# Kernel tuning notes

Measured on AMD Instinct MI355X. Metric: run time of the kernel, lower is better.

## Reference

```python
import jax, jax.numpy as jnp
import numpy as np

B, N, FIN, FOUT, H = 4, 2048, 256, 256, 4
D = FOUT // H  # out_per_head


def setup_inputs() -> dict:
    key = jax.random.key(0)
    k1, k2, k3, k4 = jax.random.split(key, 4)
    h = jax.random.normal(k1, (B, N, FIN), dtype=jnp.float32)
    adj = jax.random.randint(k2, (B, N, N), 0, 2, dtype=jnp.int32)
    idx = jnp.arange(N)
    adj = adj.at[:, idx, idx].set(1)  # self-loops: avoid empty softmax rows
    W = jax.random.normal(k3, (FOUT, FIN), dtype=jnp.float32) / np.sqrt(FIN)
    attn = jax.random.normal(k4, (H, 2 * D), dtype=jnp.float32) * 0.1
    return {"h": h, "adj": adj, "W": W, "attn": attn}


def reference(h, adj, W, attn):
    Bb, Nn, _ = h.shape
    Hh = attn.shape[0]
    d = attn.shape[1] // 2
    # h_proj: [B, H, N, d]  (nn.Linear with no bias: h @ W.T)
    hp = (h @ W.T).reshape(Bb, Nn, Hh, d).transpose(0, 2, 1, 3)
    # attn . concat(h_i, h_j) == (a_src . h_i) + (a_dst . h_j); avoids O(N^2 * 2d) concat
    a_src, a_dst = attn[:, :d], attn[:, d:]
    s = jnp.einsum('bhnd,hd->bhn', hp, a_src)  # score contribution of row node i
    t = jnp.einsum('bhnd,hd->bhn', hp, a_dst)  # score contribution of col node j
    e = jax.nn.leaky_relu(s[:, :, :, None] + t[:, :, None, :], negative_slope=0.2)
    e = jnp.where(adj[:, None, :, :] != 0, e, -jnp.inf)
    alpha = jax.nn.softmax(e, axis=-1)  # [B, H, N, N]
    h_new = jnp.einsum('bhij,bhjd->bhid', alpha, hp)
    h_new = h_new.transpose(0, 2, 1, 3).reshape(Bb, Nn, Hh * d)
    return h_new, alpha.mean(axis=1)
```

## Files before the change

### kernel.cpp

```cpp
#include <hip/hip_runtime.h>
#include <math.h>

typedef unsigned long long u64;
typedef unsigned short ushort_t;
typedef float f32x4 __attribute__((ext_vector_type(4)));
typedef short short8 __attribute__((ext_vector_type(8)));

#define BB 4
#define NN 2048
#define FINE 256
#define FOUTE 256
#define HH 4
#define DD 64
#define NW 32
#define L2E 1.44269504088896340736f

#define EXP2F(x) __builtin_amdgcn_exp2f(x)
#define LOG2F(x) __builtin_amdgcn_logf(x)

__device__ __forceinline__ float lrelu(float x) { return fmaxf(x, 0.2f * x); }

__device__ __forceinline__ unsigned short f2bf(float x) {
  unsigned u = __float_as_uint(x);
  unsigned r = u + 0x7FFFu + ((u >> 16) & 1u);
  return (unsigned short)(r >> 16);
}

__device__ __forceinline__ unsigned cvtpk(float lo, float hi) {
  unsigned r;
  asm("v_cvt_pk_bf16_f32 %0, %1, %2" : "=v"(r) : "v"(lo), "v"(hi));
  return r;
}

__global__ __launch_bounds__(256) void k_pack(const int* __restrict__ adj, u64* __restrict__ pack,
                                              float4* __restrict__ outZero) {
  int row = blockIdx.x;
  if (row < 2048) outZero[(size_t)row * 256 + threadIdx.x] = make_float4(0.f, 0.f, 0.f, 0.f);
  int wv = threadIdx.x >> 6, ln = threadIdx.x & 63;
  const int* arow = adj + (size_t)row * NN;
  u64* prow = pack + (size_t)row * NW;
  for (int w = wv; w < NW; w += 4) {
    u64 m = __ballot(arow[(w << 6) + ln] != 0);
    if (ln == 0) prow[w] = m;
  }
}

__global__ __launch_bounds__(256) void k_gemm1(const float* __restrict__ hI, const float* __restrict__ W,
                                               const float* __restrict__ attn,
                                               ushort_t* __restrict__ hpT,
                                               float* __restrict__ sB, float* __restrict__ tB,
                                               float* __restrict__ tB4) {
  __shared__ ushort_t Ab[64 * 256];
  __shared__ ushort_t Bb[64 * 256];
  __shared__ ushort_t tT[64][72];
  int m0 = blockIdx.x * 64;
  int hh = blockIdx.y;
  int f0 = hh * 64;
  int tid = threadIdx.x;
  int w = tid >> 6, lane = tid & 63;
  int li = lane & 15, g = lane >> 4;

#pragma unroll
  for (int q = 0; q < 16; ++q) {
    int fi = (q << 8) + tid;
    int row = fi >> 6, f4 = fi & 63;
    float4 va = *(const float4*)&hI[(size_t)(m0 + row) * FINE + (f4 << 2)];
    float4 vb = *(const float4*)&W[(size_t)(f0 + row) * FINE + (f4 << 2)];
    int byteOff = (row << 9) + ((f4 << 3) ^ ((row & 7) << 4));
    *(uint2*)((char*)Ab + byteOff) = make_uint2(cvtpk(va.x, va.y), cvtpk(va.z, va.w));
    *(uint2*)((char*)Bb + byteOff) = make_uint2(cvtpk(vb.x, vb.y), cvtpk(vb.z, vb.w));
  }
  __syncthreads();

  f32x4 acc[4] = {};
  int arow = (w << 4) + li;
  int abase = arow << 9, asw = (arow & 7) << 4;
#pragma unroll
  for (int kk = 0; kk < 8; ++kk) {
    short8 a = *(const short8*)((char*)Ab + abase + (((kk << 6) + (g << 4)) ^ asw));
#pragma unroll
    for (int f = 0; f < 4; ++f) {
      int brow = (f << 4) + li;
      short8 b = *(const short8*)((char*)Bb + (brow << 9) + (((kk << 6) + (g << 4)) ^ ((brow & 7) << 4)));
      acc[f] = __builtin_amdgcn_mfma_f32_16x16x32_bf16(a, b, acc[f], 0, 0, 0);
    }
  }

  float as4[4], ad4[4];
#pragma unroll
  for (int f = 0; f < 4; ++f) {
    as4[f] = attn[(hh << 7) + (f << 4) + li] * L2E;
    ad4[f] = attn[(hh << 7) + 64 + (f << 4) + li] * L2E;
  }
  float ps[4] = {0.f, 0.f, 0.f, 0.f}, pt[4] = {0.f, 0.f, 0.f, 0.f};
#pragma unroll
  for (int f = 0; f < 4; ++f)
#pragma unroll
    for (int r = 0; r < 4; ++r) { ps[r] += acc[f][r] * as4[f]; pt[r] += acc[f][r] * ad4[f]; }
#pragma unroll
  for (int off = 1; off <= 8; off <<= 1) {
#pragma unroll
    for (int r = 0; r < 4; ++r) { ps[r] += __shfl_xor(ps[r], off); pt[r] += __shfl_xor(pt[r], off); }
  }
  int b0 = m0 >> 11, n0 = m0 & (NN - 1);
  if (li == 0) {
#pragma unroll
    for (int r = 0; r < 4; ++r) {
      int nn = n0 + (w << 4) + (g << 2) + r;
      size_t idx = (size_t)(b0 * HH + hh) * NN + nn;
      sB[idx] = ps[r]; tB[idx] = pt[r];
      tB4[((size_t)b0 * NN + nn) * 4 + hh] = pt[r];
    }
  }
#pragma unroll
  for (int f = 0; f < 4; ++f)
#pragma unroll
    for (int r = 0; r < 4; ++r)
      tT[(f << 4) + li][(w << 4) + (g << 2) + r] = f2bf(acc[f][r]);
  __syncthreads();
#pragma unroll
  for (int q = 0; q < 2; ++q) {
    int dr = (q << 5) + (tid >> 3);
    int seg = tid & 7;
    *(short8*)&hpT[((size_t)((b0 * HH + hh) << 6) + dr) * NN + n0 + (seg << 3)] =
        *(const short8*)&tT[dr][seg << 3];
  }
}

__global__ __launch_bounds__(256) void k_mls(const float* __restrict__ sB, const float* __restrict__ tB4,
                                             const u64* __restrict__ pack, float* __restrict__ cB,
                                             float* __restrict__ outMean) {
  __shared__ float4 t4s[2048];
  __shared__ float4 wpart[4];
  int tid = threadIdx.x;
  int lane = tid & 63;
  int wv = tid >> 6;
  int bbase = blockIdx.x << 3;
  int b = bbase >> 11;
  const float4* t4 = (const float4*)tB4 + (size_t)b * NN;
#pragma unroll
  for (int q = 0; q < 8; ++q) t4s[(q << 8) + tid] = t4[(q << 8) + tid];
  __syncthreads();

  float4 pm = make_float4(-1e30f, -1e30f, -1e30f, -1e30f);
#pragma unroll
  for (int q = 0; q < 8; ++q) {
    float4 tv = t4s[(wv << 9) + (q << 6) + lane];
    pm.x = fmaxf(pm.x, tv.x); pm.y = fmaxf(pm.y, tv.y);
    pm.z = fmaxf(pm.z, tv.z); pm.w = fmaxf(pm.w, tv.w);
  }
#pragma unroll
  for (int off = 32; off; off >>= 1) {
    pm.x = fmaxf(pm.x, __shfl_xor(pm.x, off));
    pm.y = fmaxf(pm.y, __shfl_xor(pm.y, off));
    pm.z = fmaxf(pm.z, __shfl_xor(pm.z, off));
    pm.w = fmaxf(pm.w, __shfl_xor(pm.w, off));
  }
  if (lane == 0) wpart[wv] = pm;
  __syncthreads();
  float4 q0 = wpart[0], q1 = wpart[1], q2 = wpart[2], q3 = wpart[3];
  float tmax[4] = {fmaxf(fmaxf(q0.x, q1.x), fmaxf(q2.x, q3.x)),
                   fmaxf(fmaxf(q0.y, q1.y), fmaxf(q2.y, q3.y)),
                   fmaxf(fmaxf(q0.z, q1.z), fmaxf(q2.z, q3.z)),
                   fmaxf(fmaxf(q0.w, q1.w), fmaxf(q2.w, q3.w))};

  int r0 = __builtin_amdgcn_readfirstlane(bbase + (wv << 1));
  const u64* p0 = pack + (size_t)(r0 + 0) * NW;
  const u64* p1 = pack + (size_t)(r0 + 1) * NW;
  float sv[2][4], Ah[2][4], Bh[2][4], mh[2][4];
#pragma unroll
  for (int r = 0; r < 2; ++r)
#pragma unroll
    for (int h = 0; h < 4; ++h) {
      float s = sB[(size_t)(b * HH + h) * NN + ((r0 + r) & (NN - 1))];
      float m = lrelu(s + tmax[h]);
      sv[r][h] = s; mh[r][h] = m; Ah[r][h] = s - m; Bh[r][h] = fmaf(0.2f, s, -m);
    }
  unsigned mr0 = 0, mr1 = 0;
  float4 ls0 = make_float4(0.f, 0.f, 0.f, 0.f), ls1 = ls0;
#pragma unroll 4
  for (int k = 0; k < NW; ++k) {
    bool b0 = (p0[k] >> lane) & 1ull, b1 = (p1[k] >> lane) & 1ull;
    mr0 |= (unsigned)b0 << k; mr1 |= (unsigned)b1 << k;
    float4 tv = t4s[(k << 6) + lane];
    ls0.x += b0 ? EXP2F(fmaxf(tv.x + Ah[0][0], fmaf(0.2f, tv.x, Bh[0][0]))) : 0.f;
    ls0.y += b0 ? EXP2F(fmaxf(tv.y + Ah[0][1], fmaf(0.2f, tv.y, Bh[0][1]))) : 0.f;
    ls0.z += b0 ? EXP2F(fmaxf(tv.z + Ah[0][2], fmaf(0.2f, tv.z, Bh[0][2]))) : 0.f;
    ls0.w += b0 ? EXP2F(fmaxf(tv.w + Ah[0][3], fmaf(0.2f, tv.w, Bh[0][3]))) : 0.f;
    ls1.x += b1 ? EXP2F(fmaxf(tv.x + Ah[1][0], fmaf(0.2f, tv.x, Bh[1][0]))) : 0.f;
    ls1.y += b1 ? EXP2F(fmaxf(tv.y + Ah[1][1], fmaf(0.2f, tv.y, Bh[1][1]))) : 0.f;
    ls1.z += b1 ? EXP2F(fmaxf(tv.z + Ah[1][2], fmaf(0.2f, tv.z, Bh[1][2]))) : 0.f;
    ls1.w += b1 ? EXP2F(fmaxf(tv.w + Ah[1][3], fmaf(0.2f, tv.w, Bh[1][3]))) : 0.f;
  }
#pragma unroll
  for (int off = 32; off; off >>= 1) {
    ls0.x += __shfl_xor(ls0.x, off); ls0.y += __shfl_xor(ls0.y, off);
    ls0.z += __shfl_xor(ls0.z, off); ls0.w += __shfl_xor(ls0.w, off);
    ls1.x += __shfl_xor(ls1.x, off); ls1.y += __shfl_xor(ls1.y, off);
    ls1.z += __shfl_xor(ls1.z, off); ls1.w += __shfl_xor(ls1.w, off);
  }
  float A2[2][4], B2[2][4];
  float lv0[4] = {ls0.x, ls0.y, ls0.z, ls0.w};
  float lv1[4] = {ls1.x, ls1.y, ls1.z, ls1.w};
#pragma unroll
  for (int h = 0; h < 4; ++h) {
    float c0 = mh[0][h] + LOG2F(lv0[h]);
    float c1 = mh[1][h] + LOG2F(lv1[h]);
    A2[0][h] = sv[0][h] - c0; B2[0][h] = fmaf(0.2f, sv[0][h], -c0);
    A2[1][h] = sv[1][h] - c1; B2[1][h] = fmaf(0.2f, sv[1][h], -c1);
    if (lane == 0) {
      cB[(size_t)(b * HH + h) * NN + ((r0 + 0) & (NN - 1))] = c0;
      cB[(size_t)(b * HH + h) * NN + ((r0 + 1) & (NN - 1))] = c1;
    }
  }
#pragma unroll 2
  for (int k = 0; k < NW; ++k) {
    float4 tv = t4s[(k << 6) + lane];
    float tvv[4] = {tv.x, tv.y, tv.z, tv.w};
    float a0 = 0.f, a1 = 0.f;
#pragma unroll
    for (int h = 0; h < 4; ++h) {
      a0 += EXP2F(fmaxf(tvv[h] + A2[0][h], fmaf(0.2f, tvv[h], B2[0][h])));
      a1 += EXP2F(fmaxf(tvv[h] + A2[1][h], fmaf(0.2f, tvv[h], B2[1][h])));
    }
    outMean[(size_t)(r0 + 0) * NN + (k << 6) + lane] = ((mr0 >> k) & 1u) ? 0.25f * a0 : 0.0f;
    outMean[(size_t)(r0 + 1) * NN + (k << 6) + lane] = ((mr1 >> k) & 1u) ? 0.25f * a1 : 0.0f;
  }
}

__global__ __launch_bounds__(256) void k_pv(const ushort_t* __restrict__ hpT,
                                            const float* __restrict__ sB, const float* __restrict__ cB,
                                            const float* __restrict__ tB, const u64* __restrict__ pack,
                                            float* __restrict__ out) {
  __shared__ ushort_t hpTile[2][4096];
  int blk = blockIdx.x;
  int jh = blockIdx.y;
  int it = blk & 31, bh = blk >> 5;
  int b = bh >> 2, hh = bh & 3;
  int i0 = it << 6;
  int tid = threadIdx.x;
  int w = tid >> 6, lane = tid & 63;
  int li = lane & 15, g = lane >> 4;
  int irow = i0 + (w << 4) + li;
  float sI = sB[(size_t)bh * NN + irow];
  float cI = cB[(size_t)bh * NN + irow];
  float A0 = sI - cI, B0 = fmaf(0.2f, sI, -cI);
  const u64* packRow = pack + ((size_t)b * NN + irow) * NW;
  const float* tRow = tB + (size_t)bh * NN;

  int drow0 = (w << 4) + (lane >> 3);
  int xslot = (lane & 7) ^ (lane >> 3);
  const ushort_t* srcBase0 = hpT + ((size_t)(bh << 6) + drow0) * NN + (xslot << 3);
  const ushort_t* srcBase1 = srcBase0 + (size_t)8 * NN;

#define STAGE(buf, j0c)                                                                        \
  do {                                                                                         \
    __builtin_amdgcn_global_load_lds(                                                          \
        (const __attribute__((address_space(1))) void*)(srcBase0 + (j0c)),                     \
        (__attribute__((address_space(3))) void*)&hpTile[buf][(w << 10)], 16, 0, 0);           \
    __builtin_amdgcn_global_load_lds(                                                          \
        (const __attribute__((address_space(1))) void*)(srcBase1 + (j0c)),                     \
        (__attribute__((address_space(3))) void*)&hpTile[buf][(w << 10) + 512], 16, 0, 0);     \
  } while (0)

  f32x4 acc[4] = {};
  int jc0 = jh << 4;
  STAGE(0, jc0 << 6);
  STAGE(1, (jc0 + 1) << 6);
  float4 ta0, ta1, tb0, tb1;
  u64 wbits;
  {
    const float4* tp4 = (const float4*)(tRow + (jc0 << 6) + (g << 3));
    ta0 = tp4[0]; ta1 = tp4[1]; tb0 = tp4[8]; tb1 = tp4[9];
    wbits = packRow[jc0];
  }
  int cur = 0;

  for (int jc = jc0; jc < jc0 + 16; ++jc) {
    float tva[8] = {ta0.x, ta0.y, ta0.z, ta0.w, ta1.x, ta1.y, ta1.z, ta1.w};
    float tvb[8] = {tb0.x, tb0.y, tb0.z, tb0.w, tb1.x, tb1.y, tb1.z, tb1.w};
    unsigned bits0 = (unsigned)(wbits >> (g << 3));
    unsigned bits1 = (unsigned)(wbits >> (32 + (g << 3)));
    float ea[8], eb[8];
#pragma unroll
    for (int jj = 0; jj < 8; ++jj) {
      float e0 = EXP2F(fmaxf(tva[jj] + A0, fmaf(0.2f, tva[jj], B0)));
      ea[jj] = ((bits0 >> jj) & 1u) ? e0 : 0.0f;
      float e1 = EXP2F(fmaxf(tvb[jj] + A0, fmaf(0.2f, tvb[jj], B0)));
      eb[jj] = ((bits1 >> jj) & 1u) ? e1 : 0.0f;
    }
    uint4 ua, ub;
    ua.x = cvtpk(ea[0], ea[1]); ua.y = cvtpk(ea[2], ea[3]);
    ua.z = cvtpk(ea[4], ea[5]); ua.w = cvtpk(ea[6], ea[7]);
    ub.x = cvtpk(eb[0], eb[1]); ub.y = cvtpk(eb[2], eb[3]);
    ub.z = cvtpk(eb[4], eb[5]); ub.w = cvtpk(eb[6], eb[7]);
    short8 a0 = __builtin_bit_cast(short8, ua);
    short8 a1 = __builtin_bit_cast(short8, ub);

    if (jc < jc0 + 15) {
      const float4* tp4 = (const float4*)(tRow + ((jc + 1) << 6) + (g << 3));
      ta0 = tp4[0]; ta1 = tp4[1]; tb0 = tp4[8]; tb1 = tp4[9];
      wbits = packRow[jc + 1];
    }

    asm volatile("" ::: "memory");
    __builtin_amdgcn_sched_barrier(0);
    __builtin_amdgcn_s_barrier();
    __builtin_amdgcn_sched_barrier(0);

    const char* tile = (const char*)hpTile[cur];
#pragma unroll
    for (int f = 0; f < 4; ++f) {
      int dr = (f << 4) + li;
      int ro = dr << 7;
      int sw = (dr & 7) << 4;
      short8 b0 = *(const short8*)(tile + ro + ((g << 4) ^ sw));
      short8 b1 = *(const short8*)(tile + ro + ((64 + (g << 4)) ^ sw));
      acc[f] = __builtin_amdgcn_mfma_f32_16x16x32_bf16(a0, b0, acc[f], 0, 0, 0);
      acc[f] = __builtin_amdgcn_mfma_f32_16x16x32_bf16(a1, b1, acc[f], 0, 0, 0);
    }

    asm volatile("s_waitcnt lgkmcnt(0)" ::: "memory");
    __builtin_amdgcn_sched_barrier(0);
    __builtin_amdgcn_s_barrier();

    if (jc + 2 < jc0 + 16) STAGE(cur, (jc + 2) << 6);
    cur ^= 1;
  }
#undef STAGE

#pragma unroll
  for (int f = 0; f < 4; ++f)
#pragma unroll
    for (int r = 0; r < 4; ++r) {
      int i = i0 + (w << 4) + (g << 2) + r;
      int d = (f << 4) + li;
      atomicAdd(&out[((size_t)(b * NN + i)) * FOUTE + (hh << 6) + d], acc[f][r]);
    }
}

extern "C" void kernel_launch(void* const* d_in, const int* in_sizes, int n_in,
                              void* d_out, int out_size, void* d_ws, size_t ws_size,
                              hipStream_t stream) {
  const float* hIn  = (const float*)d_in[0];
  const int*   adj  = (const int*)d_in[1];
  const float* W    = (const float*)d_in[2];
  const float* attn = (const float*)d_in[3];
  float* out = (float*)d_out;
  float* outMean = out + (size_t)BB * NN * FOUTE;

  ushort_t* hpT = (ushort_t*)d_ws;
  float* sB  = (float*)(hpT + (size_t)BB * HH * DD * NN);
  float* tB  = sB + BB * HH * NN;
  float* cB  = tB + BB * HH * NN;
  float* tB4 = cB + BB * HH * NN;
  u64* pack  = (u64*)(tB4 + BB * HH * NN);

  hipLaunchKernelGGL(k_pack,  dim3(BB * NN), dim3(256), 0, stream, adj, pack, (float4*)out);
  hipLaunchKernelGGL(k_gemm1, dim3((BB * NN) / 64, HH), dim3(256), 0, stream, hIn, W, attn, hpT, sB, tB, tB4);
  hipLaunchKernelGGL(k_mls,   dim3((BB * NN) / 8), dim3(256), 0, stream, sB, tB4, pack, cB, outMean);
  hipLaunchKernelGGL(k_pv,    dim3(BB * HH * (NN / 64), 2), dim3(256), 0, stream, hpT, sB, cB, tB, pack, out);
}
```

Measured before the change: 96.00 us.

## Merge adjacency packing into GEMM kernel and stage t scores in LDS

Measured after the change: 123.0 us. +28.1%, slower.

```diff
diff --git a/kernel.cpp b/kernel.cpp
--- a/kernel.cpp
+++ b/kernel.cpp
@@ -32,31 +32,35 @@
   return r;
 }
 
-__global__ __launch_bounds__(256) void k_pack(const int* __restrict__ adj, u64* __restrict__ pack,
-                                              float4* __restrict__ outZero) {
-  int row = blockIdx.x;
-  if (row < 2048) outZero[(size_t)row * 256 + threadIdx.x] = make_float4(0.f, 0.f, 0.f, 0.f);
-  int wv = threadIdx.x >> 6, ln = threadIdx.x & 63;
-  const int* arow = adj + (size_t)row * NN;
-  u64* prow = pack + (size_t)row * NW;
-  for (int w = wv; w < NW; w += 4) {
-    u64 m = __ballot(arow[(w << 6) + ln] != 0);
-    if (ln == 0) prow[w] = m;
-  }
-}
-
-__global__ __launch_bounds__(256) void k_gemm1(const float* __restrict__ hI, const float* __restrict__ W,
-                                               const float* __restrict__ attn,
-                                               ushort_t* __restrict__ hpT,
-                                               float* __restrict__ sB, float* __restrict__ tB,
-                                               float* __restrict__ tB4) {
+__global__ __launch_bounds__(256) void k_pg(const float* __restrict__ hI, const float* __restrict__ W,
+                                            const float* __restrict__ attn,
+                                            ushort_t* __restrict__ hpT,
+                                            float* __restrict__ sB, float* __restrict__ tB,
+                                            float* __restrict__ tB4,
+                                            const int* __restrict__ adj, u64* __restrict__ pack,
+                                            float4* __restrict__ outZero) {
   __shared__ ushort_t Ab[64 * 256];
   __shared__ ushort_t Bb[64 * 256];
   __shared__ ushort_t tT[64][72];
-  int m0 = blockIdx.x * 64;
+  int bx = blockIdx.x;
+  int tid = threadIdx.x;
+
+  if (bx >= 128) {
+    int row = ((bx - 128) << 2) | blockIdx.y;
+    if (row < 2048) outZero[(size_t)row * 256 + tid] = make_float4(0.f, 0.f, 0.f, 0.f);
+    int wv = tid >> 6, ln = tid & 63;
+    const int* arow = adj + (size_t)row * NN;
+    u64* prow = pack + (size_t)row * NW;
+    for (int w = wv; w < NW; w += 4) {
+      u64 m = __ballot(arow[(w << 6) + ln] != 0);
+      if (ln == 0) prow[w] = m;
+    }
+    return;
+  }
+
+  int m0 = bx * 64;
   int hh = blockIdx.y;
   int f0 = hh * 64;
-  int tid = threadIdx.x;
   int w = tid >> 6, lane = tid & 63;
   int li = lane & 15, g = lane >> 4;
 
@@ -233,6 +237,7 @@
                                             const float* __restrict__ tB, const u64* __restrict__ pack,
                                             float* __restrict__ out) {
   __shared__ ushort_t hpTile[2][4096];
+  __shared__ float4 tLds[256];
   int blk = blockIdx.x;
   int jh = blockIdx.y;
   int it = blk & 31, bh = blk >> 5;
@@ -267,16 +272,14 @@
   int jc0 = jh << 4;
   STAGE(0, jc0 << 6);
   STAGE(1, (jc0 + 1) << 6);
-  float4 ta0, ta1, tb0, tb1;
-  u64 wbits;
-  {
-    const float4* tp4 = (const float4*)(tRow + (jc0 << 6) + (g << 3));
-    ta0 = tp4[0]; ta1 = tp4[1]; tb0 = tp4[8]; tb1 = tp4[9];
-    wbits = packRow[jc0];
-  }
+  tLds[tid] = ((const float4*)(tRow + (jc0 << 6)))[tid];
+  u64 wbits = packRow[jc0];
+  __syncthreads();
   int cur = 0;
 
   for (int jc = jc0; jc < jc0 + 16; ++jc) {
+    const float4* tq = tLds + ((jc - jc0) << 4) + (g << 1);
+    float4 ta0 = tq[0], ta1 = tq[1], tb0 = tq[8], tb1 = tq[9];
     float tva[8] = {ta0.x, ta0.y, ta0.z, ta0.w, ta1.x, ta1.y, ta1.z, ta1.w};
     float tvb[8] = {tb0.x, tb0.y, tb0.z, tb0.w, tb1.x, tb1.y, tb1.z, tb1.w};
     unsigned bits0 = (unsigned)(wbits >> (g << 3));
@@ -297,11 +300,7 @@
     short8 a0 = __builtin_bit_cast(short8, ua);
     short8 a1 = __builtin_bit_cast(short8, ub);
 
-    if (jc < jc0 + 15) {
-      const float4* tp4 = (const float4*)(tRow + ((jc + 1) << 6) + (g << 3));
-      ta0 = tp4[0]; ta1 = tp4[1]; tb0 = tp4[8]; tb1 = tp4[9];
-      wbits = packRow[jc + 1];
-    }
+    if (jc < jc0 + 15) wbits = packRow[jc + 1];
 
     asm volatile("" ::: "memory");
     __builtin_amdgcn_sched_barrier(0);
@@ -356,8 +355,8 @@
   float* tB4 = cB + BB * HH * NN;
   u64* pack  = (u64*)(tB4 + BB * HH * NN);
 
-  hipLaunchKernelGGL(k_pack,  dim3(BB * NN), dim3(256), 0, stream, adj, pack, (float4*)out);
-  hipLaunchKernelGGL(k_gemm1, dim3((BB * NN) / 64, HH), dim3(256), 0, stream, hIn, W, attn, hpT, sB, tB, tB4);
-  hipLaunchKernelGGL(k_mls,   dim3((BB * NN) / 8), dim3(256), 0, stream, sB, tB4, pack, cB, outMean);
-  hipLaunchKernelGGL(k_pv,    dim3(BB * HH * (NN / 64), 2), dim3(256), 0, stream, hpT, sB, cB, tB, pack, out);
-}
+  hipLaunchKernelGGL(k_pg,  dim3(128 + 2048, HH), dim3(256), 0, stream,
+                     hIn, W, attn, hpT, sB, tB, tB4, adj, pack, (float4*)out);
+  hipLaunchKernelGGL(k_mls, dim3((BB * NN) / 8), dim3(256), 0, stream, sB, tB4, pack, cB, outMean);
+  hipLaunchKernelGGL(k_pv,  dim3(BB * HH * (NN / 64), 2), dim3(256), 0, stream, hpT, sB, cB, tB, pack, out);
+}
```
